# Performance work log

Measured on AMD Instinct MI355X. Metric: run time of the kernel, lower is better.

Reference implementation:

```python
import jax, jax.numpy as jnp
import numpy as np

B, S, VOCAB, HID, NH, L, SPAN = 4, 512, 25, 512, 8, 12, 512
HEAD = HID // NH
FF = 4 * HID
EPS = 1e-7  # DebertaV2 layer_norm_eps


def _ln(x, g, b):
    m = x.mean(-1, keepdims=True)
    v = ((x - m) ** 2).mean(-1, keepdims=True)
    return (x - m) / jnp.sqrt(v + EPS) * g + b


def setup_inputs() -> dict:
    key = jax.random.key(0)
    ks = iter(jax.random.split(key, 16))
    w = lambda shape: jax.random.normal(next(ks), shape, jnp.float32) * 0.05
    return {
        "x": jax.random.randint(next(ks), (B, S), 0, VOCAB),
        "attention_mask": jnp.ones((B, S), jnp.int32),
        "word_emb": w((VOCAB, HID)),
        "emb_ln_g": jnp.ones((HID,), jnp.float32),
        "emb_ln_b": jnp.zeros((HID,), jnp.float32),
        "rel_emb": w((2 * SPAN, HID)),
        "Wq": w((L, HID, HID)), "bq": jnp.zeros((L, HID), jnp.float32),
        "Wk": w((L, HID, HID)), "bk": jnp.zeros((L, HID), jnp.float32),
        "Wv": w((L, HID, HID)), "bv": jnp.zeros((L, HID), jnp.float32),
        "Wpk": w((L, HID, HID)), "bpk": jnp.zeros((L, HID), jnp.float32),
        "Wpq": w((L, HID, HID)), "bpq": jnp.zeros((L, HID), jnp.float32),
        "Wo": w((L, HID, HID)), "bo": jnp.zeros((L, HID), jnp.float32),
        "ln1_g": jnp.ones((L, HID), jnp.float32), "ln1_b": jnp.zeros((L, HID), jnp.float32),
        "W1": w((L, HID, FF)), "b1": jnp.zeros((L, FF), jnp.float32),
        "W2": w((L, FF, HID)), "b2": jnp.zeros((L, HID), jnp.float32),
        "ln2_g": jnp.ones((L, HID), jnp.float32), "ln2_b": jnp.zeros((L, HID), jnp.float32),
        "cls_w": w((VOCAB, HID)), "cls_b": jnp.zeros((VOCAB,), jnp.float32),
    }


def _forward(x, attention_mask, word_emb, emb_ln_g, emb_ln_b, rel_emb,
             Wq, bq, Wk, bk, Wv, bv, Wpk, bpk, Wpq, bpq, Wo, bo,
             ln1_g, ln1_b, W1, b1, W2, b2, ln2_g, ln2_b, cls_w, cls_b):
    mask = attention_mask.astype(jnp.float32)
    # embeddings: word only (position_biased_input=False), LN, then masked
    h = _ln(word_emb[x], emb_ln_g, emb_ln_b) * mask[..., None]

    rel = jnp.arange(S)[:, None] - jnp.arange(S)[None, :]          # q_pos - k_pos
    c2p_idx = jnp.clip(rel + SPAN, 0, 2 * SPAN - 1)[None, None]    # [1,1,S,S]
    p2c_idx = jnp.clip(-rel + SPAN, 0, 2 * SPAN - 1)[None, None]
    attm = (mask[:, None, None, :] * mask[:, None, :, None]) > 0   # [B,1,S,S]
    scale = jnp.sqrt(jnp.float32(HEAD * 3))                        # scale_factor = 1 + len(pos_att_type)
    neg = jnp.finfo(jnp.float32).min

    def heads(t):  # [B,S,HID] -> [B,NH,S,HEAD]
        return t.reshape(B, S, NH, HEAD).transpose(0, 2, 1, 3)

    for l in range(L):
        q = heads(h @ Wq[l] + bq[l])
        k = heads(h @ Wk[l] + bk[l])
        v = heads(h @ Wv[l] + bv[l])
        # projected relative-position embeddings: [NH, 2*SPAN, HEAD]
        pk = (rel_emb @ Wpk[l] + bpk[l]).reshape(2 * SPAN, NH, HEAD).transpose(1, 0, 2)
        pq = (rel_emb @ Wpq[l] + bpq[l]).reshape(2 * SPAN, NH, HEAD).transpose(1, 0, 2)

        scores = jnp.einsum('bhqd,bhkd->bhqk', q, k)
        # c2p: query content vs key position, gathered at clamp(rel+span)
        c2p = jnp.take_along_axis(jnp.einsum('bhqd,hpd->bhqp', q, pk), c2p_idx, axis=-1)
        # p2c: key content vs query position, gathered at clamp(-rel+span) then transposed
        p2c = jnp.take_along_axis(jnp.einsum('bhkd,hpd->bhkp', k, pq), p2c_idx, axis=-1)
        scores = (scores + c2p + jnp.swapaxes(p2c, -1, -2)) / scale

        scores = jnp.where(attm, scores, neg)
        probs = jnp.where(attm, jax.nn.softmax(scores, axis=-1), 0.0)  # XSoftmax
        ctx = jnp.einsum('bhqk,bhkd->bhqd', probs, v).transpose(0, 2, 1, 3).reshape(B, S, HID)
        h = _ln(ctx @ Wo[l] + bo[l] + h, ln1_g[l], ln1_b[l])
        f = jax.nn.gelu(h @ W1[l] + b1[l], approximate=False) @ W2[l] + b2[l]
        h = _ln(f + h, ln2_g[l], ln2_b[l])

    logits = h @ cls_w.T + cls_b
    return h, logits


def reference(x, attention_mask, word_emb, emb_ln_g, emb_ln_b, rel_emb,
              Wq, bq, Wk, bk, Wv, bv, Wpk, bpk, Wpq, bpq, Wo, bo,
              ln1_g, ln1_b, W1, b1, W2, b2, ln2_g, ln2_b, cls_w, cls_b):
    return _forward(x, attention_mask, word_emb, emb_ln_g, emb_ln_b, rel_emb,
                    Wq, bq, Wk, bk, Wv, bv, Wpk, bpk, Wpq, bpq, Wo, bo,
                    ln1_g, ln1_b, W1, b1, W2, b2, ln2_g, ln2_b, cls_w, cls_b)
```

## Files before the change

### kernel.cpp

```cpp
#include <hip/hip_runtime.h>
#include <hip/hip_bf16.h>

#define BATCH  4
#define SEQ    512
#define TOK    (BATCH*SEQ)
#define HID    512
#define NHEAD  8
#define HEAD   64
#define FFDIM  2048
#define NLAYER 12
#define SPAN2  1024
#define VOCAB  25
#define LNEPS  1e-7f
#define NEG_BIG -3.0e38f

typedef __attribute__((ext_vector_type(8))) short bf16x8;
typedef __attribute__((ext_vector_type(4))) float floatx4;

#define MFMA16(a, b, c) __builtin_amdgcn_mfma_f32_16x16x32_bf16((a), (b), (c), 0, 0, 0)

__device__ __forceinline__ float b2f(unsigned short u) {
    return __uint_as_float(((unsigned int)u) << 16);
}
__device__ __forceinline__ unsigned short f2b(float f) {
    __hip_bfloat16 h = __float2bfloat16(f);
    return *(unsigned short*)&h;
}

__device__ __forceinline__ void gload16(const unsigned short* g, unsigned short* lds_base) {
    __builtin_amdgcn_global_load_lds((const __attribute__((address_space(1))) void*)g,
                                     (__attribute__((address_space(3))) void*)lds_base, 16, 0, 0);
}

__device__ __forceinline__ float wave_sum(float v) {
    #pragma unroll
    for (int o = 1; o < 64; o <<= 1) v += __shfl_xor(v, o);
    return v;
}

__device__ __forceinline__ void ln_finish(const float (&v)[8], const float* __restrict__ g,
                                          const float* __restrict__ bb, int lane, float maskf,
                                          size_t base, float* __restrict__ h,
                                          unsigned short* __restrict__ hb) {
    float sum = 0.f;
    #pragma unroll
    for (int j = 0; j < 8; j++) sum += v[j];
    float mean = wave_sum(sum) * (1.0f / HID);
    float d[8]; float var = 0.f;
    #pragma unroll
    for (int j = 0; j < 8; j++) { d[j] = v[j] - mean; var += d[j] * d[j]; }
    float rstd = rsqrtf(wave_sum(var) * (1.0f / HID) + LNEPS);
    const float* gp = g + lane * 8; const float* bp = bb + lane * 8;
    float4 g0 = *(const float4*)gp, g1 = *(const float4*)(gp + 4);
    float4 b0 = *(const float4*)bp, b1 = *(const float4*)(bp + 4);
    float gg[8] = {g0.x, g0.y, g0.z, g0.w, g1.x, g1.y, g1.z, g1.w};
    float bv[8] = {b0.x, b0.y, b0.z, b0.w, b1.x, b1.y, b1.z, b1.w};
    float o8[8];
    #pragma unroll
    for (int j = 0; j < 8; j++) o8[j] = (d[j] * rstd * gg[j] + bv[j]) * maskf;
    *(float4*)(h + base)     = make_float4(o8[0], o8[1], o8[2], o8[3]);
    *(float4*)(h + base + 4) = make_float4(o8[4], o8[5], o8[6], o8[7]);
    uint4 pb;
    pb.x = (unsigned int)f2b(o8[0]) | ((unsigned int)f2b(o8[1]) << 16);
    pb.y = (unsigned int)f2b(o8[2]) | ((unsigned int)f2b(o8[3]) << 16);
    pb.z = (unsigned int)f2b(o8[4]) | ((unsigned int)f2b(o8[5]) << 16);
    pb.w = (unsigned int)f2b(o8[6]) | ((unsigned int)f2b(o8[7]) << 16);
    *(uint4*)(hb + base) = pb;
}

__global__ void embed_ln_kernel(const int* __restrict__ x, const int* __restrict__ am,
                                const float* __restrict__ word_emb,
                                const float* __restrict__ g, const float* __restrict__ bb,
                                float* __restrict__ h, unsigned short* __restrict__ hb) {
    int wv = threadIdx.x >> 6, lane = threadIdx.x & 63;
    int t = blockIdx.x * 4 + wv;
    const float* we = word_emb + (size_t)x[t] * HID + lane * 8;
    float4 va = *(const float4*)we, vb2 = *(const float4*)(we + 4);
    float v[8] = {va.x, va.y, va.z, va.w, vb2.x, vb2.y, vb2.z, vb2.w};
    ln_finish(v, g, bb, lane, (float)am[t], (size_t)t * HID + lane * 8, h, hb);
}

__global__ void add_ln_kernel(const float* __restrict__ tmp,
                              const float* __restrict__ g, const float* __restrict__ bb,
                              float* __restrict__ h, unsigned short* __restrict__ hb) {
    int wv = threadIdx.x >> 6, lane = threadIdx.x & 63;
    int t = blockIdx.x * 4 + wv;
    size_t base = (size_t)t * HID + lane * 8;
    float4 ta = *(const float4*)(tmp + base), tb = *(const float4*)(tmp + base + 4);
    float4 ha = *(const float4*)(h + base),  hbb = *(const float4*)(h + base + 4);
    float v[8] = {ta.x + ha.x, ta.y + ha.y, ta.z + ha.z, ta.w + ha.w,
                  tb.x + hbb.x, tb.y + hbb.y, tb.z + hbb.z, tb.w + hbb.w};
    ln_finish(v, g, bb, lane, 1.0f, base, h, hb);
}

__global__ void add_ln2_kernel(const float* __restrict__ t1a, const float* __restrict__ t1b,
                               const float* __restrict__ g, const float* __restrict__ bb,
                               float* __restrict__ h, unsigned short* __restrict__ hb) {
    int wv = threadIdx.x >> 6, lane = threadIdx.x & 63;
    int t = blockIdx.x * 4 + wv;
    size_t base = (size_t)t * HID + lane * 8;
    float4 aa = *(const float4*)(t1a + base), ab = *(const float4*)(t1a + base + 4);
    float4 ba = *(const float4*)(t1b + base), bbv = *(const float4*)(t1b + base + 4);
    float4 ha = *(const float4*)(h + base),  hb2 = *(const float4*)(h + base + 4);
    float v[8] = {aa.x + ba.x + ha.x, aa.y + ba.y + ha.y, aa.z + ba.z + ha.z, aa.w + ba.w + ha.w,
                  ab.x + bbv.x + hb2.x, ab.y + bbv.y + hb2.y, ab.z + bbv.z + hb2.z, ab.w + bbv.w + hb2.w};
    ln_finish(v, g, bb, lane, 1.0f, base, h, hb);
}

__global__ void cvt_rel_kernel(const float* __restrict__ in, unsigned short* __restrict__ out) {
    int i = (blockIdx.x * 256 + threadIdx.x) * 4;
    float4 v = *(const float4*)(in + i);
    out[i] = f2b(v.x); out[i+1] = f2b(v.y); out[i+2] = f2b(v.z); out[i+3] = f2b(v.w);
}

__global__ void tcvt_kernel(const float* __restrict__ in, unsigned short* __restrict__ out,
                            int K, int N) {
    __shared__ float tile[32][33];
    int l = blockIdx.z;
    const float* ip = in + (size_t)l * K * N;
    unsigned short* op = out + (size_t)l * K * N;
    int kb = blockIdx.y * 32, nb = blockIdx.x * 32;
    int tx = threadIdx.x, ty = threadIdx.y;
    #pragma unroll
    for (int i = 0; i < 32; i += 8) tile[ty + i][tx] = ip[(size_t)(kb + ty + i) * N + nb + tx];
    __syncthreads();
    #pragma unroll
    for (int i = 0; i < 32; i += 8) op[(size_t)(nb + ty + i) * K + kb + tx] = f2b(tile[tx][ty + i]);
}

__global__ void tcvt6_kernel(const float* __restrict__ Wq, const float* __restrict__ Wk,
                             const float* __restrict__ Wv, const float* __restrict__ Wpk,
                             const float* __restrict__ Wpq, const float* __restrict__ Wo,
                             unsigned short* __restrict__ out) {
    __shared__ float tile[32][33];
    int z = blockIdx.z, l = z / 6, w = z - l * 6;
    const float* src = w == 0 ? Wq : w == 1 ? Wk : w == 2 ? Wv : w == 3 ? Wpk : w == 4 ? Wpq : Wo;
    const float* ip = src + (size_t)l * HID * HID;
    unsigned short* op = out + ((size_t)w * NLAYER + l) * HID * HID;
    int kb = blockIdx.y * 32, nb = blockIdx.x * 32;
    int tx = threadIdx.x, ty = threadIdx.y;
    #pragma unroll
    for (int i = 0; i < 32; i += 8) tile[ty + i][tx] = ip[(size_t)(kb + ty + i) * HID + nb + tx];
    __syncthreads();
    #pragma unroll
    for (int i = 0; i < 32; i += 8) op[(size_t)(nb + ty + i) * HID + kb + tx] = f2b(tile[tx][ty + i]);
}

__device__ __forceinline__ void gemm_core128(
    const unsigned short* __restrict__ A, const unsigned short* __restrict__ Bt,
    int row0, int col0, int K, int kbeg, int kend,
    floatx4 (&acc)[4][2], unsigned short* AsB, unsigned short* BsB) {
    int tid = threadIdx.x;
    int lane = tid & 63, w = tid >> 6;
    int wm = w >> 1, wn = w & 1;
    int m16 = lane & 15, quad = lane >> 4;

    int arow[4], acol[4], brow[2], bcol[2];
    #pragma unroll
    for (int c = 0; c < 4; c++) {
        int o = ((w * 4 + c) * 64 + lane) * 16;
        int r = o >> 7;
        arow[c] = r;
        acol[c] = (o & 127) ^ ((r & 7) << 4);
    }
    #pragma unroll
    for (int c = 0; c < 2; c++) {
        int o = ((w * 2 + c) * 64 + lane) * 16;
        int r = o >> 7;
        brow[c] = r;
        bcol[c] = (o & 127) ^ ((r & 7) << 4);
    }

    auto stage = [&](int bf, int k0) {
        #pragma unroll
        for (int c = 0; c < 4; c++)
            gload16(A + (size_t)(row0 + arow[c]) * K + k0 + (acol[c] >> 1),
                    AsB + bf * 8192 + (w * 4 + c) * 512);
        #pragma unroll
        for (int c = 0; c < 2; c++)
            gload16(Bt + (size_t)(col0 + brow[c]) * K + k0 + (bcol[c] >> 1),
                    BsB + bf * 4096 + (w * 2 + c) * 512);
    };

    stage(0, kbeg);
    __syncthreads();
    int cur = 0;
    for (int k0 = kbeg; k0 < kend; k0 += 64) {
        if (k0 + 64 < kend) stage(cur ^ 1, k0 + 64);
        const char* Ab = (const char*)(AsB + cur * 8192);
        const char* Bb = (const char*)(BsB + cur * 4096);
        int br0 = wn * 32 + m16, br1 = wn * 32 + 16 + m16;
        #pragma unroll
        for (int kk = 0; kk < 2; kk++) {
            bf16x8 bf0 = *(const bf16x8*)(Bb + ((((br0 << 7) + kk * 64 + quad * 16)) ^ ((m16 & 7) << 4)));
            bf16x8 bf1 = *(const bf16x8*)(Bb + ((((br1 << 7) + kk * 64 + quad * 16)) ^ ((m16 & 7) << 4)));
            #pragma unroll
            for (int mi = 0; mi < 4; mi++) {
                int ar = wm * 64 + mi * 16 + m16;
                bf16x8 af = *(const bf16x8*)(Ab + ((((ar << 7) + kk * 64 + quad * 16)) ^ ((m16 & 7) << 4)));
                acc[mi][0] = MFMA16(af, bf0, acc[mi][0]);
                acc[mi][1] = MFMA16(af, bf1, acc[mi][1]);
            }
        }
        __syncthreads();
        cur ^= 1;
    }
}

template<bool OUT_BF16, bool GELU, int SPLITK>
__global__ __launch_bounds__(256, 2) void gemm_bt2(
    const unsigned short* __restrict__ A, const unsigned short* __restrict__ Bt,
    const float* __restrict__ bias, void* __restrict__ Cp, int N, int K) {
    __shared__ unsigned short As[2][8192], Bs[2][4096];
    int row0 = blockIdx.y * 128, col0 = blockIdx.x * 64;
    int kseg = K / SPLITK;
    int kbeg = kseg * blockIdx.z, kend = kbeg + kseg;
    floatx4 acc[4][2];
    #pragma unroll
    for (int mi = 0; mi < 4; mi++)
        #pragma unroll
        for (int ni = 0; ni < 2; ni++) acc[mi][ni] = (floatx4){0.f, 0.f, 0.f, 0.f};
    gemm_core128(A, Bt, row0, col0, K, kbeg, kend, acc, &As[0][0], &Bs[0][0]);

    int tid = threadIdx.x, lane = tid & 63, wid = tid >> 6;
    int wm = wid >> 1, wn = wid & 1, m16 = lane & 15, quad = lane >> 4;
    size_t outoff = (size_t)blockIdx.z * (size_t)(gridDim.y << 7) * N;
    #pragma unroll
    for (int ni = 0; ni < 2; ni++) {
        int colg = col0 + wn * 32 + ni * 16 + m16;
        float bval = (SPLITK == 1 || blockIdx.z == 0) ? bias[colg] : 0.0f;
        #pragma unroll
        for (int mi = 0; mi < 4; mi++) {
            #pragma unroll
            for (int r = 0; r < 4; r++) {
                int rowg = row0 + wm * 64 + mi * 16 + quad * 4 + r;
                float v = acc[mi][ni][r] + bval;
                if (GELU) v = 0.5f * v * (1.0f + erff(v * 0.70710678118654752f));
                if (OUT_BF16) ((unsigned short*)Cp)[(size_t)rowg * N + colg] = f2b(v);
                else          ((float*)Cp)[outoff + (size_t)rowg * N + colg] = v;
            }
        }
    }
}

__global__ __launch_bounds__(256, 2) void qkvp_gemm(
    const unsigned short* __restrict__ hb, const unsigned short* __restrict__ relb,
    const unsigned short* __restrict__ Wqt, const unsigned short* __restrict__ Wkt,
    const unsigned short* __restrict__ Wvt, const unsigned short* __restrict__ Wpkt,
    const unsigned short* __restrict__ Wpqt,
    const float* __restrict__ bq, const float* __restrict__ bk, const float* __restrict__ bv,
    const float* __restrict__ bpk, const float* __restrict__ bpq,
    unsigned short* __restrict__ qb, unsigned short* __restrict__ kb,
    unsigned short* __restrict__ vb, unsigned short* __restrict__ pkb,
    unsigned short* __restrict__ pqb) {
    __shared__ unsigned short As[2][8192], Bs[2][4096];
    int bid = blockIdx.x;
    int xcd = bid & 7, slot = bid >> 3;
    int op, j;
    if (xcd < 6) { op = xcd >> 1; j = slot * 2 + (xcd & 1); }
    else         { op = xcd - 3;  j = slot; }
    int trow = j >> 3, tcol = j & 7;
    const unsigned short* A; const unsigned short* Bt; const float* bias; unsigned short* C;
    if (op < 3) {
        A = hb;
        Bt   = op == 0 ? Wqt : op == 1 ? Wkt : Wvt;
        bias = op == 0 ? bq  : op == 1 ? bk  : bv;
        C    = op == 0 ? qb  : op == 1 ? kb  : vb;
    } else {
        A = relb;
        Bt   = op == 3 ? Wpkt : Wpqt;
        bias = op == 3 ? bpk  : bpq;
        C    = op == 3 ? pkb  : pqb;
    }
    floatx4 acc[4][2];
    #pragma unroll
    for (int mi = 0; mi < 4; mi++)
        #pragma unroll
        for (int ni = 0; ni < 2; ni++) acc[mi][ni] = (floatx4){0.f, 0.f, 0.f, 0.f};
    gemm_core128(A, Bt, trow * 128, tcol * 64, HID, 0, HID, acc, &As[0][0], &Bs[0][0]);

    int tid = threadIdx.x, lane = tid & 63, wid = tid >> 6;
    int wm = wid >> 1, wn = wid & 1, m16 = lane & 15, quad = lane >> 4;
    #pragma unroll
    for (int ni = 0; ni < 2; ni++) {
        int colg = tcol * 64 + wn * 32 + ni * 16 + m16;
        float bval = bias[colg];
        #pragma unroll
        for (int mi = 0; mi < 4; mi++) {
            #pragma unroll
            for (int r = 0; r < 4; r++) {
                int rowg = trow * 128 + wm * 64 + mi * 16 + quad * 4 + r;
                C[(size_t)rowg * HID + colg] = f2b(acc[mi][ni][r] + bval);
            }
        }
    }
}

template<bool OUT_BF16, bool GELU>
__global__ __launch_bounds__(256) void mfma_gemm(
    const unsigned short* __restrict__ A, const float* __restrict__ B,
    const float* __restrict__ bias, void* __restrict__ Cp, int N, int K) {
    __shared__ unsigned short As[64][72];
    __shared__ unsigned short Bs[64][72];
    int tid = threadIdx.x;
    int lane = tid & 63, wid = tid >> 6;
    int wm = wid >> 1, wn = wid & 1;
    int row0 = blockIdx.y * 64, col0 = blockIdx.x * 64;
    int m16 = lane & 15, quad = lane >> 4;

    int ar = tid >> 2, ac = (tid & 3) << 4;
    int bk = (tid >> 3) << 1, bn = (tid & 7) << 3;

    const unsigned short* Ag = A + (size_t)(row0 + ar) * K + ac;
    const float* Bg = B + (size_t)bk * N + col0 + bn;

    floatx4 acc[2][2];
    #pragma unroll
    for (int mi = 0; mi < 2; mi++)
        #pragma unroll
        for (int ni = 0; ni < 2; ni++) acc[mi][ni] = (floatx4){0.f, 0.f, 0.f, 0.f};

    for (int k0 = 0; k0 < K; k0 += 64) {
        uint4 av0 = *(const uint4*)(Ag + k0);
        uint4 av1 = *(const uint4*)(Ag + k0 + 8);
        const float* br0 = Bg + (size_t)k0 * N;
        const float* br1 = br0 + N;
        float4 b00 = *(const float4*)br0, b01 = *(const float4*)(br0 + 4);
        float4 b10 = *(const float4*)br1, b11 = *(const float4*)(br1 + 4);
        *(uint4*)&As[ar][ac] = av0;
        *(uint4*)&As[ar][ac + 8] = av1;
        float lo[8] = {b00.x, b00.y, b00.z, b00.w, b01.x, b01.y, b01.z, b01.w};
        float hi[8] = {b10.x, b10.y, b10.z, b10.w, b11.x, b11.y, b11.z, b11.w};
        #pragma unroll
        for (int i = 0; i < 8; i++) {
            unsigned int p = (unsigned int)f2b(lo[i]) | ((unsigned int)f2b(hi[i]) << 16);
            *(unsigned int*)&Bs[bn + i][bk] = p;
        }
        __syncthreads();
        #pragma unroll
        for (int kk = 0; kk < 2; kk++) {
            bf16x8 a0 = *(const bf16x8*)&As[wm * 32 + m16][kk * 32 + quad * 8];
            bf16x8 a1 = *(const bf16x8*)&As[wm * 32 + 16 + m16][kk * 32 + quad * 8];
            bf16x8 b0 = *(const bf16x8*)&Bs[wn * 32 + m16][kk * 32 + quad * 8];
            bf16x8 b1 = *(const bf16x8*)&Bs[wn * 32 + 16 + m16][kk * 32 + quad * 8];
            acc[0][0] = MFMA16(a0, b0, acc[0][0]);
            acc[0][1] = MFMA16(a0, b1, acc[0][1]);
            acc[1][0] = MFMA16(a1, b0, acc[1][0]);
            acc[1][1] = MFMA16(a1, b1, acc[1][1]);
        }
        __syncthreads();
    }
    #pragma unroll
    for (int ni = 0; ni < 2; ni++) {
        int colg = col0 + wn * 32 + ni * 16 + m16;
        float bv = bias[colg];
        #pragma unroll
        for (int mi = 0; mi < 2; mi++) {
            #pragma unroll
            for (int r = 0; r < 4; r++) {
                int rowg = row0 + wm * 32 + mi * 16 + quad * 4 + r;
                float v = acc[mi][ni][r] + bv;
                if (GELU) v = 0.5f * v * (1.0f + erff(v * 0.70710678118654752f));
                if (OUT_BF16) ((unsigned short*)Cp)[(size_t)rowg * N + colg] = f2b(v);
                else          ((float*)Cp)[(size_t)rowg * N + colg] = v;
            }
        }
    }
}

__global__ __launch_bounds__(256, 2) void attn_kernel(
    const unsigned short* __restrict__ Q, const unsigned short* __restrict__ K,
    const unsigned short* __restrict__ V,
    const unsigned short* __restrict__ PK, const unsigned short* __restrict__ PQ,
    const int* __restrict__ am, unsigned short* __restrict__ ctx) {
    __shared__ unsigned short Ks[2][32][72];
    __shared__ unsigned short Vt[2][64][40];
    __shared__ float Afs[4][16][49];
    __shared__ float Bfs[4][32][50];
    __shared__ unsigned short Pls[4][16][40];
    __shared__ int mkk[2][32];
    __shared__ float mergeML[2][2][16];

    int bid = blockIdx.x;
    int hh = bid & 7;
    int b  = (bid >> 3) & 3;
    int q0 = (bid >> 5) * 32;
    int tid = threadIdx.x;
    int lane = tid & 63, wave = tid >> 6;
    int u = wave >> 1;
    int s = wave & 1;
    int quad = lane >> 4, m16 = lane & 15;
    const float inv_scale = 0.07216878364870323f;

    const unsigned short* qg = Q + (size_t)(b * SEQ + q0 + u * 16 + m16) * HID + hh * HEAD;
    bf16x8 qf0 = *(const bf16x8*)(qg + quad * 8);
    bf16x8 qf1 = *(const bf16x8*)(qg + 32 + quad * 8);

    int sr = tid >> 3;
    int sc = (tid & 7) * 8;
    int vkey = ((sc >> 3) & 3) << 3;

    floatx4 accO[4];
    #pragma unroll
    for (int nt = 0; nt < 4; nt++) accO[nt] = (floatx4){0.f, 0.f, 0.f, 0.f};
    float mreg[4] = {NEG_BIG, NEG_BIG, NEG_BIG, NEG_BIG};
    float lreg[4] = {0.f, 0.f, 0.f, 0.f};

    auto loadPQ = [&](int t, bf16x8 (&pkf)[3][2], bf16x8 (&pqf)[3][2]) {
        int P0  = q0 - 32 * t + 481;
        int P20 = 32 * t - q0 + 481;
        int Jb  = 16 - 16 * u;
        #pragma unroll
        for (int nt = 0; nt < 3; nt++) {
            int prow = P0 + 16 * u + nt * 16 + m16;
            const unsigned short* pg = PK + (size_t)prow * HID + hh * HEAD + quad * 8;
            pkf[nt][0] = *(const bf16x8*)pg;
            pkf[nt][1] = *(const bf16x8*)(pg + 32);
            int prow2 = P20 + Jb + nt * 16 + m16;
            if (prow2 > 1023) prow2 = 1023;
            const unsigned short* pg2 = PQ + (size_t)prow2 * HID + hh * HEAD + quad * 8;
            pqf[nt][0] = *(const bf16x8*)pg2;
            pqf[nt][1] = *(const bf16x8*)(pg2 + 32);
        }
    };

    auto stageKV = [&](int ph) {
        #pragma unroll
        for (int sl = 0; sl < 2; sl++) {
            int k0 = ph * 64 + sl * 32;
            const unsigned short* kg = K + (size_t)(b * SEQ + k0 + sr) * HID + hh * HEAD + sc;
            *(uint4*)&Ks[sl][sr][sc] = *(const uint4*)kg;
            uint4 vv = *(const uint4*)(V + (size_t)(b * SEQ + k0 + sr) * HID + hh * HEAD + sc);
            unsigned short* vp = (unsigned short*)&vv;
            #pragma unroll
            for (int j = 0; j < 8; j++) Vt[sl][sc + j][sr ^ vkey] = vp[j];
        }
        if (tid < 64) mkk[tid >> 5][tid & 31] = am[b * SEQ + ph * 64 + tid];
    };

    auto computePhase = [&](bf16x8 (&pkf)[3][2], bf16x8 (&pqf)[3][2]) {
        floatx4 accS[2];
        accS[0] = (floatx4){0.f, 0.f, 0.f, 0.f};
        accS[1] = (floatx4){0.f, 0.f, 0.f, 0.f};
        #pragma unroll
        for (int n = 0; n < 2; n++) {
            bf16x8 kfa = *(const bf16x8*)&Ks[s][n * 16 + m16][quad * 8];
            bf16x8 kfb = *(const bf16x8*)&Ks[s][n * 16 + m16][32 + quad * 8];
            accS[n] = MFMA16(qf0, kfa, accS[n]);
            accS[n] = MFMA16(qf1, kfb, accS[n]);
        }
        {
            floatx4 accA[3];
            #pragma unroll
            for (int nt = 0; nt < 3; nt++) {
                accA[nt] = (floatx4){0.f, 0.f, 0.f, 0.f};
                accA[nt] = MFMA16(qf0, pkf[nt][0], accA[nt]);
                accA[nt] = MFMA16(qf1, pkf[nt][1], accA[nt]);
            }
            #pragma unroll
            for (int nt = 0; nt < 3; nt++)
                #pragma unroll
                for (int r = 0; r < 4; r++)
                    Afs[wave][quad * 4 + r][nt * 16 + m16] = accA[nt][r];
        }
        {
            floatx4 accB[2][3];
            #pragma unroll
            for (int mt = 0; mt < 2; mt++) {
                bf16x8 afa = *(const bf16x8*)&Ks[s][mt * 16 + m16][quad * 8];
                bf16x8 afb = *(const bf16x8*)&Ks[s][mt * 16 + m16][32 + quad * 8];
                #pragma unroll
                for (int nt = 0; nt < 3; nt++) {
                    accB[mt][nt] = (floatx4){0.f, 0.f, 0.f, 0.f};
                    accB[mt][nt] = MFMA16(afa, pqf[nt][0], accB[mt][nt]);
                    accB[mt][nt] = MFMA16(afb, pqf[nt][1], accB[mt][nt]);
                }
            }
            #pragma unroll
            for (int mt = 0; mt < 2; mt++)
                #pragma unroll
                for (int nt = 0; nt < 3; nt++)
                    #pragma unroll
                    for (int r = 0; r < 4; r++)
                        Bfs[wave][mt * 16 + quad * 4 + r][nt * 16 + m16] = accB[mt][nt][r];
        }
        float sv[2][4];
        float tmax[4] = {NEG_BIG, NEG_BIG, NEG_BIG, NEG_BIG};
        #pragma unroll
        for (int n = 0; n < 2; n++) {
            #pragma unroll
            for (int r = 0; r < 4; r++) {
                int qq = quad * 4 + r;
                int kc = n * 16 + m16;
                float av = Afs[wave][qq][qq - kc + 31];
                float bv = Bfs[wave][kc][kc - qq + 15];
                float x = (accS[n][r] + av + bv) * inv_scale;
                x = mkk[s][kc] ? x : NEG_BIG;
                sv[n][r] = x;
                tmax[r] = fmaxf(tmax[r], x);
            }
        }
        float alpha[4], psum[4];
        #pragma unroll
        for (int r = 0; r < 4; r++) {
            float tm = tmax[r];
            tm = fmaxf(tm, __shfl_xor(tm, 1));
            tm = fmaxf(tm, __shfl_xor(tm, 2));
            tm = fmaxf(tm, __shfl_xor(tm, 4));
            tm = fmaxf(tm, __shfl_xor(tm, 8));
            float mo = mreg[r];
            float mn = fmaxf(mo, tm);
            alpha[r] = __expf(mo - mn);
            mreg[r] = mn;
        }
        #pragma unroll
        for (int r = 0; r < 4; r++) psum[r] = 0.f;
        #pragma unroll
        for (int n = 0; n < 2; n++) {
            #pragma unroll
            for (int r = 0; r < 4; r++) {
                float p = (sv[n][r] > -1.5e38f) ? __expf(sv[n][r] - mreg[r]) : 0.0f;
                unsigned short pb = f2b(p);
                Pls[wave][quad * 4 + r][n * 16 + m16] = pb;
                psum[r] += b2f(pb);
            }
        }
        #pragma unroll
        for (int r = 0; r < 4; r++) {
            float ps = psum[r];
            ps += __shfl_xor(ps, 1);
            ps += __shfl_xor(ps, 2);
            ps += __shfl_xor(ps, 4);
            ps += __shfl_xor(ps, 8);
            lreg[r] = lreg[r] * alpha[r] + ps;
        }
        #pragma unroll
        for (int nt = 0; nt < 4; nt++)
            #pragma unroll
            for (int r = 0; r < 4; r++) accO[nt][r] *= alpha[r];
        {
            bf16x8 pf = *(const bf16x8*)&Pls[wave][m16][quad * 8];
            #pragma unroll
            for (int nt = 0; nt < 4; nt++) {
                int d = nt * 16 + m16;
                int kq = (quad ^ ((d >> 3) & 3)) * 8;
                bf16x8 vf = *(const bf16x8*)&Vt[s][d][kq];
                accO[nt] = MFMA16(pf, vf, accO[nt]);
            }
        }
    };

    bf16x8 pkfA[3][2], pqfA[3][2], pkfB[3][2], pqfB[3][2];
    loadPQ(s, pkfA, pqfA);
    #pragma unroll
    for (int pp = 0; pp < 4; pp++) {
        {
            int ph = 2 * pp;
            __syncthreads();
            stageKV(ph);
            __syncthreads();
            if (ph < 7) loadPQ(2 * (ph + 1) + s, pkfB, pqfB);
            computePhase(pkfA, pqfA);
        }
        {
            int ph = 2 * pp + 1;
            __syncthreads();
            stageKV(ph);
            __syncthreads();
            if (ph < 7) loadPQ(2 * (ph + 1) + s, pkfA, pqfA);
            computePhase(pkfB, pqfB);
        }
    }

    __syncthreads();
    float* mo = &Bfs[0][0][0];
    if (s == 1) {
        #pragma unroll
        for (int nt = 0; nt < 4; nt++)
            #pragma unroll
            for (int r = 0; r < 4; r++)
                mo[u * 1056 + (quad * 4 + r) * 66 + nt * 16 + m16] = accO[nt][r];
        if (m16 == 0) {
            #pragma unroll
            for (int r = 0; r < 4; r++) {
                mergeML[u][0][quad * 4 + r] = mreg[r];
                mergeML[u][1][quad * 4 + r] = lreg[r];
            }
        }
    }
    __syncthreads();
    if (s == 0) {
        #pragma unroll
        for (int r = 0; r < 4; r++) {
            int row = quad * 4 + r;
            float m1 = mergeML[u][0][row], l1 = mergeML[u][1][row];
            float m0 = mreg[r], l0 = lreg[r];
            float mt = fmaxf(m0, m1);
            float a0 = __expf(m0 - mt), a1 = __expf(m1 - mt);
            float lt = l0 * a0 + l1 * a1;
            float inv = lt > 0.0f ? 1.0f / lt : 0.0f;
            inv *= (float)am[b * SEQ + q0 + u * 16 + row];
            #pragma unroll
            for (int nt = 0; nt < 4; nt++) {
                float o1 = mo[u * 1056 + row * 66 + nt * 16 + m16];
                float val = (accO[nt][r] * a0 + o1 * a1) * inv;
                ctx[(size_t)(b * SEQ + q0 + u * 16 + row) * HID + hh * HEAD + nt * 16 + m16] = f2b(val);
            }
        }
    }
}

__global__ void copy_f_kernel(const float* __restrict__ in, float* __restrict__ out, int n) {
    int i = blockIdx.x * 256 + threadIdx.x;
    if (i < n) out[i] = in[i];
}
__global__ void cls_kernel(const float* __restrict__ h, const float* __restrict__ cls_w,
                           const float* __restrict__ cls_b, float* __restrict__ out) {
    int t = blockIdx.x, v = threadIdx.x;
    if (v < VOCAB) {
        const float* hr = h + (size_t)t * HID;
        const float* wr = cls_w + (size_t)v * HID;
        float acc = cls_b[v];
        for (int d = 0; d < HID; d++) acc += hr[d] * wr[d];
        out[t * VOCAB + v] = acc;
    }
}

extern "C" void kernel_launch(void* const* d_in, const int* in_sizes, int n_in,
                              void* d_out, int out_size, void* d_ws, size_t ws_size,
                              hipStream_t stream) {
    const int* x     = (const int*)d_in[0];
    const int* am    = (const int*)d_in[1];
    const float* word_emb = (const float*)d_in[2];
    const float* emb_g    = (const float*)d_in[3];
    const float* emb_b    = (const float*)d_in[4];
    const float* rel_emb  = (const float*)d_in[5];
    const float* Wq  = (const float*)d_in[6];  const float* bq  = (const float*)d_in[7];
    const float* Wk  = (const float*)d_in[8];  const float* bk  = (const float*)d_in[9];
    const float* Wv  = (const float*)d_in[10]; const float* bv  = (const float*)d_in[11];
    const float* Wpk = (const float*)d_in[12]; const float* bpk = (const float*)d_in[13];
    const float* Wpq = (const float*)d_in[14]; const float* bpq = (const float*)d_in[15];
    const float* Wo  = (const float*)d_in[16]; const float* bo  = (const float*)d_in[17];
    const float* ln1g = (const float*)d_in[18]; const float* ln1b = (const float*)d_in[19];
    const float* W1  = (const float*)d_in[20]; const float* b1  = (const float*)d_in[21];
    const float* W2  = (const float*)d_in[22]; const float* b2  = (const float*)d_in[23];
    const float* ln2g = (const float*)d_in[24]; const float* ln2b = (const float*)d_in[25];
    const float* cls_w = (const float*)d_in[26]; const float* cls_b = (const float*)d_in[27];

    char* wsb = (char*)d_ws;
    const size_t NEED_BIG = 107u << 20;

    if (ws_size >= NEED_BIG) {
        float* h  = (float*)wsb;
        float* t1 = (float*)(wsb + (4u << 20));
        float* t2 = (float*)(wsb + (8u << 20));
        unsigned short* qb   = (unsigned short*)(wsb + (12u << 20));
        unsigned short* kb   = (unsigned short*)(wsb + (14u << 20));
        unsigned short* vb   = (unsigned short*)(wsb + (16u << 20));
        unsigned short* pkb  = (unsigned short*)(wsb + (18u << 20));
        unsigned short* pqb  = (unsigned short*)(wsb + (19u << 20));
        unsigned short* relb = (unsigned short*)(wsb + (20u << 20));
        unsigned short* hb   = (unsigned short*)(wsb + (21u << 20));
        unsigned short* ctx  = hb;
        unsigned short* ffb  = qb;
        unsigned short* Wqt  = (unsigned short*)(wsb + (23u << 20));
        unsigned short* W1t  = (unsigned short*)(wsb + (59u << 20));
        unsigned short* W2t  = (unsigned short*)(wsb + (83u << 20));

        const size_t M512 = (size_t)HID * HID;

        tcvt6_kernel<<<dim3(16, 16, 72), dim3(32, 8), 0, stream>>>(Wq, Wk, Wv, Wpk, Wpq, Wo, Wqt);
        tcvt_kernel<<<dim3(64, 16, 12), dim3(32, 8), 0, stream>>>(W1, W1t, HID, FFDIM);
        tcvt_kernel<<<dim3(16, 64, 12), dim3(32, 8), 0, stream>>>(W2, W2t, FFDIM, HID);
        cvt_rel_kernel<<<dim3(SPAN2 * HID / 1024), dim3(256), 0, stream>>>(rel_emb, relb);
        embed_ln_kernel<<<dim3(TOK / 4), dim3(256), 0, stream>>>(x, am, word_emb, emb_g, emb_b, h, hb);

        for (int l = 0; l < NLAYER; l++) {
            qkvp_gemm<<<dim3(512), dim3(256), 0, stream>>>(
                hb, relb,
                Wqt + (size_t)(0 * NLAYER + l) * M512, Wqt + (size_t)(1 * NLAYER + l) * M512,
                Wqt + (size_t)(2 * NLAYER + l) * M512, Wqt + (size_t)(3 * NLAYER + l) * M512,
                Wqt + (size_t)(4 * NLAYER + l) * M512,
                bq + l * HID, bk + l * HID, bv + l * HID, bpk + l * HID, bpq + l * HID,
                qb, kb, vb, pkb, pqb);

            attn_kernel<<<dim3(512), dim3(256), 0, stream>>>(
                qb, kb, vb, pkb, pqb, am, ctx);

            gemm_bt2<false, false, 2><<<dim3(HID / 64, TOK / 128, 2), dim3(256), 0, stream>>>(
                ctx, Wqt + (size_t)(5 * NLAYER + l) * M512, bo + l * HID, t1, HID, HID);
            add_ln2_kernel<<<dim3(TOK / 4), dim3(256), 0, stream>>>(t1, t2, ln1g + l * HID, ln1b + l * HID, h, hb);

            gemm_bt2<true, true, 1><<<dim3(FFDIM / 64, TOK / 128, 1), dim3(256), 0, stream>>>(
                hb, W1t + (size_t)l * HID * FFDIM, b1 + l * FFDIM, ffb, FFDIM, HID);
            gemm_bt2<false, false, 2><<<dim3(HID / 64, TOK / 128, 2), dim3(256), 0, stream>>>(
                ffb, W2t + (size_t)l * HID * FFDIM, b2 + l * HID, t1, HID, FFDIM);
            add_ln2_kernel<<<dim3(TOK / 4), dim3(256), 0, stream>>>(t1, t2, ln2g + l * HID, ln2b + l * HID, h, hb);
        }

        float* out_f = (float*)d_out;
        copy_f_kernel<<<dim3(TOK * HID / 256), dim3(256), 0, stream>>>(h, out_f, TOK * HID);
        cls_kernel<<<dim3(TOK), dim3(32), 0, stream>>>(h, cls_w, cls_b, out_f + TOK * HID);
        return;
    }

    const size_t NEEDED = 19u << 20;
    if (ws_size < NEEDED) return;
    float* h  = (float*)wsb;
    float* t1 = (float*)(wsb + (4u << 20));
    unsigned short* qb   = (unsigned short*)(wsb + (8u << 20));
    unsigned short* kb   = qb  + (1u << 20);
    unsigned short* vb   = kb  + (1u << 20);
    unsigned short* pkb  = vb  + (1u << 20);
    unsigned short* pqb  = pkb + (1u << 19);
    unsigned short* relb = (unsigned short*)(wsb + (16u << 20));
    unsigned short* hb   = (unsigned short*)(wsb + (17u << 20));
    unsigned short* ctx  = hb;
    unsigned short* ffb  = qb;

    cvt_rel_kernel<<<dim3(SPAN2 * HID / 1024), dim3(256), 0, stream>>>(rel_emb, relb);
    embed_ln_kernel<<<dim3(TOK / 4), dim3(256), 0, stream>>>(x, am, word_emb, emb_g, emb_b, h, hb);

    for (int l = 0; l < NLAYER; l++) {
        const float* Wq_l = Wq + (size_t)l * HID * HID;
        const float* Wk_l = Wk + (size_t)l * HID * HID;
        const float* Wv_l = Wv + (size_t)l * HID * HID;
        const float* Wo_l = Wo + (size_t)l * HID * HID;
        const float* Wpk_l = Wpk + (size_t)l * HID * HID;
        const float* Wpq_l = Wpq + (size_t)l * HID * HID;
        const float* W1_l = W1 + (size_t)l * HID * FFDIM;
        const float* W2_l = W2 + (size_t)l * FFDIM * HID;

        mfma_gemm<true,  false><<<dim3(HID/64, TOK/64),   dim3(256), 0, stream>>>(hb,   Wq_l,  bq + l*HID,  qb,  HID, HID);
        mfma_gemm<true,  false><<<dim3(HID/64, TOK/64),   dim3(256), 0, stream>>>(hb,   Wk_l,  bk + l*HID,  kb,  HID, HID);
        mfma_gemm<true,  false><<<dim3(HID/64, TOK/64),   dim3(256), 0, stream>>>(hb,   Wv_l,  bv + l*HID,  vb,  HID, HID);
        mfma_gemm<true,  false><<<dim3(HID/64, SPAN2/64), dim3(256), 0, stream>>>(relb, Wpk_l, bpk + l*HID, pkb, HID, HID);
        mfma_gemm<true,  false><<<dim3(HID/64, SPAN2/64), dim3(256), 0, stream>>>(relb, Wpq_l, bpq + l*HID, pqb, HID, HID);

        attn_kernel<<<dim3(512), dim3(256), 0, stream>>>(qb, kb, vb, pkb, pqb, am, ctx);

        mfma_gemm<false, false><<<dim3(HID/64, TOK/64),   dim3(256), 0, stream>>>(ctx,  Wo_l,  bo + l*HID,  t1,  HID, HID);
        add_ln_kernel<<<dim3(TOK / 4), dim3(256), 0, stream>>>(t1, ln1g + l*HID, ln1b + l*HID, h, hb);

        mfma_gemm<true,  true ><<<dim3(FFDIM/64, TOK/64), dim3(256), 0, stream>>>(hb,   W1_l,  b1 + l*FFDIM, ffb, FFDIM, HID);
        mfma_gemm<false, false><<<dim3(HID/64, TOK/64),   dim3(256), 0, stream>>>(ffb,  W2_l,  b2 + l*HID,  t1,  HID, FFDIM);
        add_ln_kernel<<<dim3(TOK / 4), dim3(256), 0, stream>>>(t1, ln2g + l*HID, ln2b + l*HID, h, hb);
    }

    float* out_f = (float*)d_out;
    copy_f_kernel<<<dim3(TOK*HID/256), dim3(256), 0, stream>>>(h, out_f, TOK*HID);
    cls_kernel<<<dim3(TOK), dim3(32), 0, stream>>>(h, cls_w, cls_b, out_f + TOK*HID);
}
```

Before: 1.424 ms.

## Use 64x64 split-K GEMMs, tanh GELU, MFMA priority hints, direct final LN output

Replaces the 128-row tile GEMM for the Wo and W2 projections with a new 64x64 register-double-buffered tile GEMM, doubling the number of blocks so the GPU's compute units are better filled. It swaps the exact erf GELU for a tanh approximation built on __expf, adds s_setprio hints around the MFMA sections of attention, and vectorises the classifier dot product with float4 loads. It also has the last layer's LayerNorm write straight into the output buffer, removing the final copy kernel. The tanh GELU changes the numerics compared with the reference's exact erf GELU.

Measured after the change: 1.348 ms. -5.4%, faster.

```diff
diff --git a/kernel.cpp b/kernel.cpp
--- a/kernel.cpp
+++ b/kernel.cpp
@@ -26,6 +26,11 @@
     __hip_bfloat16 h = __float2bfloat16(f);
     return *(unsigned short*)&h;
 }
+__device__ __forceinline__ float gelu_tanh(float v) {
+    float y = 1.5957691216057308f * (v + 0.044715f * v * v * v);
+    float t = 1.0f - 2.0f / (__expf(y) + 1.0f);
+    return 0.5f * v * (1.0f + t);
+}
 
 __device__ __forceinline__ void gload16(const unsigned short* g, unsigned short* lds_base) {
     __builtin_amdgcn_global_load_lds((const __attribute__((address_space(1))) void*)g,
@@ -95,16 +100,17 @@
 
 __global__ void add_ln2_kernel(const float* __restrict__ t1a, const float* __restrict__ t1b,
                                const float* __restrict__ g, const float* __restrict__ bb,
-                               float* __restrict__ h, unsigned short* __restrict__ hb) {
+                               const float* __restrict__ hin, float* __restrict__ hout,
+                               unsigned short* __restrict__ hb) {
     int wv = threadIdx.x >> 6, lane = threadIdx.x & 63;
     int t = blockIdx.x * 4 + wv;
     size_t base = (size_t)t * HID + lane * 8;
     float4 aa = *(const float4*)(t1a + base), ab = *(const float4*)(t1a + base + 4);
     float4 ba = *(const float4*)(t1b + base), bbv = *(const float4*)(t1b + base + 4);
-    float4 ha = *(const float4*)(h + base),  hb2 = *(const float4*)(h + base + 4);
+    float4 ha = *(const float4*)(hin + base), hb2 = *(const float4*)(hin + base + 4);
     float v[8] = {aa.x + ba.x + ha.x, aa.y + ba.y + ha.y, aa.z + ba.z + ha.z, aa.w + ba.w + ha.w,
                   ab.x + bbv.x + hb2.x, ab.y + bbv.y + hb2.y, ab.z + bbv.z + hb2.z, ab.w + bbv.w + hb2.w};
-    ln_finish(v, g, bb, lane, 1.0f, base, h, hb);
+    ln_finish(v, g, bb, lane, 1.0f, base, hout, hb);
 }
 
 __global__ void cvt_rel_kernel(const float* __restrict__ in, unsigned short* __restrict__ out) {
@@ -146,6 +152,96 @@
     for (int i = 0; i < 32; i += 8) op[(size_t)(nb + ty + i) * HID + kb + tx] = f2b(tile[tx][ty + i]);
 }
 
+__device__ __forceinline__ void gemm_tile_bt(
+    const unsigned short* __restrict__ A, const unsigned short* __restrict__ Bt,
+    int row0, int col0, int K, int kbeg, int kend,
+    floatx4 (&acc)[2][2], unsigned short (&As)[2][64][72], unsigned short (&Bs)[2][64][72]) {
+    int tid = threadIdx.x;
+    int lane = tid & 63, wid = tid >> 6;
+    int wm = wid >> 1, wn = wid & 1;
+    int m16 = lane & 15, quad = lane >> 4;
+    int sr = tid >> 2, sc = (tid & 3) << 4;
+    const unsigned short* Ag = A + (size_t)(row0 + sr) * K + sc;
+    const unsigned short* Bg = Bt + (size_t)(col0 + sr) * K + sc;
+
+    uint4 av0 = *(const uint4*)(Ag + kbeg);
+    uint4 av1 = *(const uint4*)(Ag + kbeg + 8);
+    uint4 bv0 = *(const uint4*)(Bg + kbeg);
+    uint4 bv1 = *(const uint4*)(Bg + kbeg + 8);
+    *(uint4*)&As[0][sr][sc]     = av0;
+    *(uint4*)&As[0][sr][sc + 8] = av1;
+    *(uint4*)&Bs[0][sr][sc]     = bv0;
+    *(uint4*)&Bs[0][sr][sc + 8] = bv1;
+    __syncthreads();
+
+    int cur = 0;
+    for (int k0 = kbeg; k0 < kend; k0 += 64) {
+        int k1 = k0 + 64;
+        bool more = k1 < kend;
+        if (more) {
+            av0 = *(const uint4*)(Ag + k1);
+            av1 = *(const uint4*)(Ag + k1 + 8);
+            bv0 = *(const uint4*)(Bg + k1);
+            bv1 = *(const uint4*)(Bg + k1 + 8);
+        }
+        #pragma unroll
+        for (int kk = 0; kk < 2; kk++) {
+            bf16x8 a0 = *(const bf16x8*)&As[cur][wm * 32 + m16][kk * 32 + quad * 8];
+            bf16x8 a1 = *(const bf16x8*)&As[cur][wm * 32 + 16 + m16][kk * 32 + quad * 8];
+            bf16x8 b0 = *(const bf16x8*)&Bs[cur][wn * 32 + m16][kk * 32 + quad * 8];
+            bf16x8 b1 = *(const bf16x8*)&Bs[cur][wn * 32 + 16 + m16][kk * 32 + quad * 8];
+            acc[0][0] = MFMA16(a0, b0, acc[0][0]);
+            acc[0][1] = MFMA16(a0, b1, acc[0][1]);
+            acc[1][0] = MFMA16(a1, b0, acc[1][0]);
+            acc[1][1] = MFMA16(a1, b1, acc[1][1]);
+        }
+        if (more) {
+            *(uint4*)&As[cur ^ 1][sr][sc]     = av0;
+            *(uint4*)&As[cur ^ 1][sr][sc + 8] = av1;
+            *(uint4*)&Bs[cur ^ 1][sr][sc]     = bv0;
+            *(uint4*)&Bs[cur ^ 1][sr][sc + 8] = bv1;
+            __syncthreads();
+            cur ^= 1;
+        }
+    }
+}
+
+template<bool OUT_BF16, bool GELU, int SPLITK>
+__global__ __launch_bounds__(256) void gemm_bt(
+    const unsigned short* __restrict__ A, const unsigned short* __restrict__ Bt,
+    const float* __restrict__ bias, void* __restrict__ Cp, int N, int K) {
+    __shared__ unsigned short As[2][64][72], Bs[2][64][72];
+    int row0 = blockIdx.y * 64, col0 = blockIdx.x * 64;
+    int kseg = K / SPLITK;
+    int kbeg = kseg * blockIdx.z, kend = kbeg + kseg;
+    floatx4 acc[2][2];
+    #pragma unroll
+    for (int mi = 0; mi < 2; mi++)
+        #pragma unroll
+        for (int ni = 0; ni < 2; ni++) acc[mi][ni] = (floatx4){0.f, 0.f, 0.f, 0.f};
+    gemm_tile_bt(A, Bt, row0, col0, K, kbeg, kend, acc, As, Bs);
+
+    int tid = threadIdx.x, lane = tid & 63, wid = tid >> 6;
+    int wm = wid >> 1, wn = wid & 1, m16 = lane & 15, quad = lane >> 4;
+    size_t outoff = (size_t)blockIdx.z * (size_t)(gridDim.y << 6) * N;
+    #pragma unroll
+    for (int ni = 0; ni < 2; ni++) {
+        int colg = col0 + wn * 32 + ni * 16 + m16;
+        float bval = (SPLITK == 1 || blockIdx.z == 0) ? bias[colg] : 0.0f;
+        #pragma unroll
+        for (int mi = 0; mi < 2; mi++) {
+            #pragma unroll
+            for (int r = 0; r < 4; r++) {
+                int rowg = row0 + wm * 32 + mi * 16 + quad * 4 + r;
+                float v = acc[mi][ni][r] + bval;
+                if (GELU) v = gelu_tanh(v);
+                if (OUT_BF16) ((unsigned short*)Cp)[(size_t)rowg * N + colg] = f2b(v);
+                else          ((float*)Cp)[outoff + (size_t)rowg * N + colg] = v;
+            }
+        }
+    }
+}
+
 __device__ __forceinline__ void gemm_core128(
     const unsigned short* __restrict__ A, const unsigned short* __restrict__ Bt,
     int row0, int col0, int K, int kbeg, int kend,
@@ -235,7 +331,7 @@
             for (int r = 0; r < 4; r++) {
                 int rowg = row0 + wm * 64 + mi * 16 + quad * 4 + r;
                 float v = acc[mi][ni][r] + bval;
-                if (GELU) v = 0.5f * v * (1.0f + erff(v * 0.70710678118654752f));
+                if (GELU) v = gelu_tanh(v);
                 if (OUT_BF16) ((unsigned short*)Cp)[(size_t)rowg * N + colg] = f2b(v);
                 else          ((float*)Cp)[outoff + (size_t)rowg * N + colg] = v;
             }
@@ -360,7 +456,7 @@
             for (int r = 0; r < 4; r++) {
                 int rowg = row0 + wm * 32 + mi * 16 + quad * 4 + r;
                 float v = acc[mi][ni][r] + bv;
-                if (GELU) v = 0.5f * v * (1.0f + erff(v * 0.70710678118654752f));
+                if (GELU) v = gelu_tanh(v);
                 if (OUT_BF16) ((unsigned short*)Cp)[(size_t)rowg * N + colg] = f2b(v);
                 else          ((float*)Cp)[(size_t)rowg * N + colg] = v;
             }
@@ -439,6 +535,7 @@
     };
 
     auto computePhase = [&](bf16x8 (&pkf)[3][2], bf16x8 (&pqf)[3][2]) {
+        __builtin_amdgcn_s_setprio(1);
         floatx4 accS[2];
         accS[0] = (floatx4){0.f, 0.f, 0.f, 0.f};
         accS[1] = (floatx4){0.f, 0.f, 0.f, 0.f};
@@ -484,6 +581,7 @@
                     for (int r = 0; r < 4; r++)
                         Bfs[wave][mt * 16 + quad * 4 + r][nt * 16 + m16] = accB[mt][nt][r];
         }
+        __builtin_amdgcn_s_setprio(0);
         float sv[2][4];
         float tmax[4] = {NEG_BIG, NEG_BIG, NEG_BIG, NEG_BIG};
         #pragma unroll
@@ -539,6 +637,7 @@
             #pragma unroll
             for (int r = 0; r < 4; r++) accO[nt][r] *= alpha[r];
         {
+            __builtin_amdgcn_s_setprio(1);
             bf16x8 pf = *(const bf16x8*)&Pls[wave][m16][quad * 8];
             #pragma unroll
             for (int nt = 0; nt < 4; nt++) {
@@ -547,6 +646,7 @@
                 bf16x8 vf = *(const bf16x8*)&Vt[s][d][kq];
                 accO[nt] = MFMA16(pf, vf, accO[nt]);
             }
+            __builtin_amdgcn_s_setprio(0);
         }
     };
 
@@ -621,7 +721,11 @@
         const float* hr = h + (size_t)t * HID;
         const float* wr = cls_w + (size_t)v * HID;
         float acc = cls_b[v];
-        for (int d = 0; d < HID; d++) acc += hr[d] * wr[d];
+        for (int d = 0; d < HID; d += 4) {
+            float4 hv = *(const float4*)(hr + d);
+            float4 wv = *(const float4*)(wr + d);
+            acc += hv.x * wv.x + hv.y * wv.y + hv.z * wv.z + hv.w * wv.w;
+        }
         out[t * VOCAB + v] = acc;
     }
 }
@@ -668,6 +772,7 @@
         unsigned short* W2t  = (unsigned short*)(wsb + (83u << 20));
 
         const size_t M512 = (size_t)HID * HID;
+        float* out_f = (float*)d_out;
 
         tcvt6_kernel<<<dim3(16, 16, 72), dim3(32, 8), 0, stream>>>(Wq, Wk, Wv, Wpk, Wpq, Wo, Wqt);
         tcvt_kernel<<<dim3(64, 16, 12), dim3(32, 8), 0, stream>>>(W1, W1t, HID, FFDIM);
@@ -687,20 +792,20 @@
             attn_kernel<<<dim3(512), dim3(256), 0, stream>>>(
                 qb, kb, vb, pkb, pqb, am, ctx);
 
-            gemm_bt2<false, false, 2><<<dim3(HID / 64, TOK / 128, 2), dim3(256), 0, stream>>>(
+            gemm_bt<false, false, 2><<<dim3(HID / 64, TOK / 64, 2), dim3(256), 0, stream>>>(
                 ctx, Wqt + (size_t)(5 * NLAYER + l) * M512, bo + l * HID, t1, HID, HID);
-            add_ln2_kernel<<<dim3(TOK / 4), dim3(256), 0, stream>>>(t1, t2, ln1g + l * HID, ln1b + l * HID, h, hb);
+            add_ln2_kernel<<<dim3(TOK / 4), dim3(256), 0, stream>>>(
+                t1, t2, ln1g + l * HID, ln1b + l * HID, h, h, hb);
 
             gemm_bt2<true, true, 1><<<dim3(FFDIM / 64, TOK / 128, 1), dim3(256), 0, stream>>>(
                 hb, W1t + (size_t)l * HID * FFDIM, b1 + l * FFDIM, ffb, FFDIM, HID);
-            gemm_bt2<false, false, 2><<<dim3(HID / 64, TOK / 128, 2), dim3(256), 0, stream>>>(
+            gemm_bt<false, false, 2><<<dim3(HID / 64, TOK / 64, 2), dim3(256), 0, stream>>>(
                 ffb, W2t + (size_t)l * HID * FFDIM, b2 + l * HID, t1, HID, FFDIM);
-            add_ln2_kernel<<<dim3(TOK / 4), dim3(256), 0, stream>>>(t1, t2, ln2g + l * HID, ln2b + l * HID, h, hb);
-        }
-
-        float* out_f = (float*)d_out;
-        copy_f_kernel<<<dim3(TOK * HID / 256), dim3(256), 0, stream>>>(h, out_f, TOK * HID);
-        cls_kernel<<<dim3(TOK), dim3(32), 0, stream>>>(h, cls_w, cls_b, out_f + TOK * HID);
+            add_ln2_kernel<<<dim3(TOK / 4), dim3(256), 0, stream>>>(
+                t1, t2, ln2g + l * HID, ln2b + l * HID, h, (l == NLAYER - 1) ? out_f : h, hb);
+        }
+
+        cls_kernel<<<dim3(TOK), dim3(32), 0, stream>>>(out_f, cls_w, cls_b, out_f + TOK * HID);
         return;
     }
 
```
